# Performance work log

Hardware: AMD Instinct MI355X
Metric: run time of the kernel (lower is better)

## Reference

```python
import jax, jax.numpy as jnp
import numpy as np

B, T, F, H, O = 4096, 64, 512, 64, 2

def setup_inputs() -> dict:
    key = jax.random.key(0)
    ks = jax.random.split(key, 7)
    s_ih = 1.0 / np.sqrt(H)
    return {
        "x": jax.random.normal(ks[0], (B, T, F), dtype=jnp.float32),
        # PyTorch LSTM params: weight_ih_l0 [4H, F], weight_hh_l0 [4H, H], biases [4H]
        "W_ih": jax.random.uniform(ks[1], (4 * H, F), jnp.float32, -s_ih, s_ih),
        "W_hh": jax.random.uniform(ks[2], (4 * H, H), jnp.float32, -s_ih, s_ih),
        "b_ih": jax.random.uniform(ks[3], (4 * H,), jnp.float32, -s_ih, s_ih),
        "b_hh": jax.random.uniform(ks[4], (4 * H,), jnp.float32, -s_ih, s_ih),
        "W_fc": jax.random.uniform(ks[5], (O, H), jnp.float32, -s_ih, s_ih),
        "b_fc": jax.random.uniform(ks[6], (O,), jnp.float32, -s_ih, s_ih),
    }

def _lstm_last_h(x, W_ih, W_hh, b_ih, b_hh):
    # Precompute input contributions for all timesteps: [B, T, 4H]
    xg = jnp.einsum('btf,gf->btg', x, W_ih) + (b_ih + b_hh)
    h0 = jnp.zeros((x.shape[0], W_hh.shape[1]), x.dtype)
    c0 = jnp.zeros_like(h0)

    def step(carry, xt):
        h, c = carry
        gates = xt + h @ W_hh.T  # [B, 4H]
        i, f, g, o = jnp.split(gates, 4, axis=-1)  # PyTorch gate order i,f,g,o
        i = jax.nn.sigmoid(i)
        f = jax.nn.sigmoid(f)
        g = jnp.tanh(g)
        o = jax.nn.sigmoid(o)
        c_new = f * c + i * g
        h_new = o * jnp.tanh(c_new)
        return (h_new, c_new), None

    (hT, _), _ = jax.lax.scan(step, (h0, c0), jnp.swapaxes(xg, 0, 1))  # scan over T
    return hT  # [B, H] = out[:, -1, :]

def reference(x, W_ih, W_hh, b_ih, b_hh, W_fc, b_fc):
    hT = _lstm_last_h(x, W_ih, W_hh, b_ih, b_hh)
    return hT @ W_fc.T + b_fc  # [B, O]
```

## Files before the change

kernel.cpp:

```cpp
#include <hip/hip_runtime.h>

#define B_SZ 4096
#define T_SZ 64
#define F_SZ 512
#define H_SZ 64
#define BR 8
#define TC 8
#define NCHUNK (T_SZ / TC)
#define NTILE 64
#define WIH_HALF_ELEMS (256 * 512)

typedef _Float16 f16x8 __attribute__((ext_vector_type(8)));
typedef float f32x4 __attribute__((ext_vector_type(4)));

__device__ __forceinline__ float fast_rcp(float x) { return __builtin_amdgcn_rcpf(x); }
__device__ __forceinline__ float sigm(float x) { return fast_rcp(1.0f + __expf(-x)); }
__device__ __forceinline__ float tanh_f(float x) {
  x = fminf(15.0f, fmaxf(-15.0f, x));
  float e = __expf(2.0f * x);
  return (e - 1.0f) * fast_rcp(e + 1.0f);
}
__device__ __forceinline__ f16x8 cvt8(float4 a, float4 b) {
  f16x8 h;
  h[0] = (_Float16)a.x; h[1] = (_Float16)a.y; h[2] = (_Float16)a.z; h[3] = (_Float16)a.w;
  h[4] = (_Float16)b.x; h[5] = (_Float16)b.y; h[6] = (_Float16)b.z; h[7] = (_Float16)b.w;
  return h;
}

__global__ void transcode_f16(const float* __restrict__ Wih, const float* __restrict__ Whh,
                              _Float16* __restrict__ ws) {
  const int i4 = (blockIdx.x * 256 + threadIdx.x) * 4;
  if (i4 < WIH_HALF_ELEMS) {
    float4 v = *(const float4*)(Wih + i4);
    ws[i4] = (_Float16)v.x; ws[i4+1] = (_Float16)v.y; ws[i4+2] = (_Float16)v.z; ws[i4+3] = (_Float16)v.w;
  } else {
    const int j4 = i4 - WIH_HALF_ELEMS;
    float4 v = *(const float4*)(Whh + j4);
    _Float16* w2 = ws + WIH_HALF_ELEMS;
    w2[j4] = (_Float16)v.x; w2[j4+1] = (_Float16)v.y; w2[j4+2] = (_Float16)v.z; w2[j4+3] = (_Float16)v.w;
  }
}

__global__ __launch_bounds__(256, 2)
void lstm_fused(const float* __restrict__ x, const _Float16* __restrict__ ws,
                const float* __restrict__ bih, const float* __restrict__ bhh,
                const float* __restrict__ Wfc, const float* __restrict__ bfc,
                float* __restrict__ out)
{
  __shared__ __align__(16) float Ax[4][64 * 64];
  __shared__ __align__(16) _Float16 hbuf[2][8][72];
  __shared__ float cb[8][64];
  __shared__ float h32[8][64];

  const int tid  = threadIdx.x;
  const int wv   = tid >> 6;
  const int lane = tid & 63;
  const int ln   = lane & 15;
  const int kg   = lane >> 4;
  const int br0  = blockIdx.x * BR;
  const int u    = wv * 16 + ln;

  const _Float16* Wihh = ws;
  const _Float16* Whhh = ws + WIH_HALF_ELEMS;

  for (int i = tid; i < 8 * 72; i += 256) (&hbuf[0][0][0])[i] = (_Float16)0.0f;
  for (int i = tid; i < 8 * 64; i += 256) (&cb[0][0])[i] = 0.0f;
  __syncthreads();

  f16x8 whhf[4][2];
  #pragma unroll
  for (int g = 0; g < 4; ++g)
    #pragma unroll
    for (int k2 = 0; k2 < 2; ++k2)
      whhf[g][k2] = *(const f16x8*)(Whhh + (size_t)((g * 4 + wv) * 16 + ln) * H_SZ
                                         + kg * 8 + k2 * 32);

  float bsum[4];
  #pragma unroll
  for (int g = 0; g < 4; ++g) bsum[g] = bih[g * 64 + u] + bhh[g * 64 + u];

  auto issue_tile = [&](int tau) {
    if (tau >= NTILE) return;
    const int cc = tau >> 3, kk = tau & 7, slot = tau & 3;
    #pragma unroll
    for (int j = 0; j < 4; ++j) {
      const int i = wv * 4 + j;
      const int m = i * 4 + (lane >> 4);
      const int kw = (((lane & 15) << 2) ^ ((m & 7) << 2));
      const float* gp = x + (size_t)(br0 + (m & 7)) * (T_SZ * F_SZ)
                          + (size_t)(cc * TC + (m >> 3)) * F_SZ + kk * 64 + kw;
      __builtin_amdgcn_global_load_lds(gp, &Ax[slot][i * 256], 16, 0, 0);
    }
  };

  auto load_bfr = [&](f16x8 (&b)[4][2], int kk) {
    #pragma unroll
    for (int g = 0; g < 4; ++g)
      #pragma unroll
      for (int k2 = 0; k2 < 2; ++k2)
        b[g][k2] = *(const f16x8*)(Wihh + (size_t)((g * 4 + wv) * 16 + ln) * F_SZ
                                        + kk * 64 + kg * 8 + k2 * 32);
  };

  f32x4 acc[4][4];
  const int sw = (ln & 7) << 2;

  auto phaseA_iter = [&](int tau, f16x8 (&bcon)[4][2], f16x8 (&bpre)[4][2]) {
    asm volatile("s_waitcnt vmcnt(16)" ::: "memory");
    __builtin_amdgcn_s_barrier();
    load_bfr(bpre, (tau + 1) & 7);
    issue_tile(tau + 3);
    asm volatile("" ::: "memory");
    const float* axs = &Ax[tau & 3][0];
    #pragma unroll
    for (int t = 0; t < 4; ++t) {
      const int rb  = (t * 16 + ln) * 64;
      const int w00 = (kg * 8) ^ sw;
      float4 a0 = *(const float4*)(axs + rb + w00);
      float4 a1 = *(const float4*)(axs + rb + (w00 ^ 4));
      float4 a2 = *(const float4*)(axs + rb + 32 + w00);
      float4 a3 = *(const float4*)(axs + rb + 32 + (w00 ^ 4));
      f16x8 af0 = cvt8(a0, a1);
      f16x8 af1 = cvt8(a2, a3);
      #pragma unroll
      for (int g = 0; g < 4; ++g) {
        acc[t][g] = __builtin_amdgcn_mfma_f32_16x16x32_f16(af0, bcon[g][0], acc[t][g], 0, 0, 0);
        acc[t][g] = __builtin_amdgcn_mfma_f32_16x16x32_f16(af1, bcon[g][1], acc[t][g], 0, 0, 0);
      }
    }
  };

  issue_tile(0); issue_tile(1); issue_tile(2);
  asm volatile("" ::: "memory");
  f16x8 bA[4][2], bB[4][2];
  load_bfr(bA, 0);

  for (int cc = 0; cc < NCHUNK; ++cc) {
    #pragma unroll
    for (int t = 0; t < 4; ++t)
      #pragma unroll
      for (int g = 0; g < 4; ++g) acc[t][g] = (f32x4){0.0f, 0.0f, 0.0f, 0.0f};

    #pragma unroll
    for (int kp = 0; kp < 4; ++kp) {
      phaseA_iter(cc * 8 + 2 * kp,     bA, bB);
      phaseA_iter(cc * 8 + 2 * kp + 1, bB, bA);
    }

    #pragma unroll
    for (int s = 0; s < TC; ++s) {
      const int st   = cc * TC + s;
      const int half = s & 1;
      f16x8 ah0 = (f16x8){0, 0, 0, 0, 0, 0, 0, 0};
      f16x8 ah1 = (f16x8){0, 0, 0, 0, 0, 0, 0, 0};
      if ((ln >> 3) == half) {
        const _Float16* hr = &hbuf[st & 1][ln & 7][0];
        ah0 = *(const f16x8*)(hr + kg * 8);
        ah1 = *(const f16x8*)(hr + kg * 8 + 32);
      }
      f32x4 gf[4];
      #pragma unroll
      for (int g = 0; g < 4; ++g) {
        gf[g] = __builtin_amdgcn_mfma_f32_16x16x32_f16(ah0, whhf[g][0], acc[s >> 1][g], 0, 0, 0);
        gf[g] = __builtin_amdgcn_mfma_f32_16x16x32_f16(ah1, whhf[g][1], gf[g], 0, 0, 0);
      }
      if ((kg >> 1) == half) {
        const int b0 = (kg & 1) * 4;
        #pragma unroll
        for (int r = 0; r < 4; ++r) {
          const float iv = sigm(gf[0][r] + bsum[0]);
          const float fv = sigm(gf[1][r] + bsum[1]);
          const float gv = tanh_f(gf[2][r] + bsum[2]);
          const float ov = sigm(gf[3][r] + bsum[3]);
          const float cn = fv * cb[b0 + r][u] + iv * gv;
          cb[b0 + r][u] = cn;
          const float hn = ov * tanh_f(cn);
          hbuf[(st + 1) & 1][b0 + r][u] = (_Float16)hn;
          if (st == T_SZ - 1) h32[b0 + r][u] = hn;
        }
      }
      asm volatile("s_waitcnt lgkmcnt(0)" ::: "memory");
      __builtin_amdgcn_s_barrier();
    }
  }

  __syncthreads();
  if (tid < 16) {
    const int r = tid >> 1, j = tid & 1;
    float a = bfc[j];
    #pragma unroll
    for (int uu = 0; uu < 64; ++uu) a += h32[r][uu] * Wfc[j * 64 + uu];
    out[(size_t)(br0 + r) * 2 + j] = a;
  }
}

extern "C" void kernel_launch(void* const* d_in, const int* in_sizes, int n_in,
                              void* d_out, int out_size, void* d_ws, size_t ws_size,
                              hipStream_t stream) {
  const float* x   = (const float*)d_in[0];
  const float* Wih = (const float*)d_in[1];
  const float* Whh = (const float*)d_in[2];
  const float* bih = (const float*)d_in[3];
  const float* bhh = (const float*)d_in[4];
  const float* Wfc = (const float*)d_in[5];
  const float* bfc = (const float*)d_in[6];
  float* out = (float*)d_out;
  _Float16* ws = (_Float16*)d_ws;

  transcode_f16<<<dim3(144), dim3(256), 0, stream>>>(Wih, Whh, ws);
  lstm_fused<<<dim3(B_SZ / BR), dim3(256), 0, stream>>>(x, ws, bih, bhh, Wfc, bfc, out);
}
```

Measured before the change: 207.2 us.

## Split fused LSTM into input-projection GEMM and a separate recurrent scan kernel

Replaces the single fused kernel with two kernels. The first computes the input projection x·W_ih^T plus bias for every batch row and timestep with MFMA and writes it to workspace in fp16, laid out time-major. The second runs the recurrence, prefetching those precomputed gates per 4-step chunk and keeping the cell state in registers. The aim is to take the large GEMM off the serial recurrence path so it runs with full parallelism, at the cost of an extra 128 MB fp16 round trip through HBM and one more launch. The old fused kernel is kept as a fallback for when the workspace is too small.

```diff
diff --git a/kernel.cpp b/kernel.cpp
--- a/kernel.cpp
+++ b/kernel.cpp
@@ -4,12 +4,11 @@
 #define T_SZ 64
 #define F_SZ 512
 #define H_SZ 64
-#define BR 8
-#define TC 8
-#define NCHUNK (T_SZ / TC)
-#define NTILE 64
-#define WIH_HALF_ELEMS (256 * 512)
-
+#define WIH_ELEMS (256 * 512)
+#define WHH_ELEMS (256 * 64)
+#define XG_ELEMS ((size_t)B_SZ * T_SZ * 256)
+
+typedef _Float16 f16x4 __attribute__((ext_vector_type(4)));
 typedef _Float16 f16x8 __attribute__((ext_vector_type(8)));
 typedef float f32x4 __attribute__((ext_vector_type(4)));
 
@@ -30,22 +29,191 @@
 __global__ void transcode_f16(const float* __restrict__ Wih, const float* __restrict__ Whh,
                               _Float16* __restrict__ ws) {
   const int i4 = (blockIdx.x * 256 + threadIdx.x) * 4;
-  if (i4 < WIH_HALF_ELEMS) {
+  if (i4 < WIH_ELEMS) {
     float4 v = *(const float4*)(Wih + i4);
     ws[i4] = (_Float16)v.x; ws[i4+1] = (_Float16)v.y; ws[i4+2] = (_Float16)v.z; ws[i4+3] = (_Float16)v.w;
   } else {
-    const int j4 = i4 - WIH_HALF_ELEMS;
+    const int j4 = i4 - WIH_ELEMS;
     float4 v = *(const float4*)(Whh + j4);
-    _Float16* w2 = ws + WIH_HALF_ELEMS;
+    _Float16* w2 = ws + WIH_ELEMS;
     w2[j4] = (_Float16)v.x; w2[j4+1] = (_Float16)v.y; w2[j4+2] = (_Float16)v.z; w2[j4+3] = (_Float16)v.w;
   }
 }
 
 __global__ __launch_bounds__(256, 2)
-void lstm_fused(const float* __restrict__ x, const _Float16* __restrict__ ws,
-                const float* __restrict__ bih, const float* __restrict__ bhh,
-                const float* __restrict__ Wfc, const float* __restrict__ bfc,
-                float* __restrict__ out)
+void xg_gemm(const float* __restrict__ x, const _Float16* __restrict__ ws,
+             const float* __restrict__ bih, const float* __restrict__ bhh,
+             _Float16* __restrict__ xg)
+{
+  __shared__ __align__(16) _Float16 A[64][520];
+
+  const int tid = threadIdx.x, wv = tid >> 6, lane = tid & 63;
+  const int ln = lane & 15, kg = lane >> 4;
+  const int b = blockIdx.x;
+  const int u = wv * 16 + ln;
+  const _Float16* Wihh = ws;
+
+  {
+    const float* src = x + (size_t)b * (T_SZ * F_SZ) + wv * 8192;
+    #pragma unroll 4
+    for (int i = 0; i < 32; ++i) {
+      float4 v = ((const float4*)src)[i * 64 + lane];
+      f16x4 h = {(_Float16)v.x, (_Float16)v.y, (_Float16)v.z, (_Float16)v.w};
+      const int m = wv * 16 + (i >> 1);
+      const int k = (i & 1) * 256 + lane * 4;
+      *(f16x4*)&A[m][k] = h;
+    }
+  }
+  float bb[4];
+  #pragma unroll
+  for (int g = 0; g < 4; ++g) bb[g] = bih[g * 64 + u] + bhh[g * 64 + u];
+  __syncthreads();
+
+  f32x4 acc[4][4];
+  #pragma unroll
+  for (int mt = 0; mt < 4; ++mt)
+    #pragma unroll
+    for (int g = 0; g < 4; ++g) acc[mt][g] = (f32x4){bb[g], bb[g], bb[g], bb[g]};
+
+  #pragma unroll 2
+  for (int kk = 0; kk < 16; ++kk) {
+    f16x8 bfr[4];
+    #pragma unroll
+    for (int g = 0; g < 4; ++g)
+      bfr[g] = *(const f16x8*)(Wihh + (size_t)((g * 4 + wv) * 16 + ln) * F_SZ + kk * 32 + kg * 8);
+    #pragma unroll
+    for (int mt = 0; mt < 4; ++mt) {
+      f16x8 af = *(const f16x8*)&A[mt * 16 + ln][kk * 32 + kg * 8];
+      #pragma unroll
+      for (int g = 0; g < 4; ++g)
+        acc[mt][g] = __builtin_amdgcn_mfma_f32_16x16x32_f16(af, bfr[g], acc[mt][g], 0, 0, 0);
+    }
+  }
+
+  __syncthreads();
+  _Float16* bn = &A[0][0];
+  #pragma unroll
+  for (int mt = 0; mt < 4; ++mt)
+    #pragma unroll
+    for (int r = 0; r < 4; ++r) {
+      f16x4 p = {(_Float16)acc[mt][0][r], (_Float16)acc[mt][1][r],
+                 (_Float16)acc[mt][2][r], (_Float16)acc[mt][3][r]};
+      *(f16x4*)(bn + (size_t)(mt * 16 + kg * 4 + r) * 264 + u * 4) = p;
+    }
+  __syncthreads();
+  {
+    const int t = tid >> 2, seg = tid & 3;
+    _Float16* dst = xg + ((size_t)t * B_SZ + b) * 256 + seg * 64;
+    const _Float16* srcb = bn + (size_t)t * 264 + seg * 64;
+    #pragma unroll
+    for (int j = 0; j < 8; ++j)
+      *(f16x8*)(dst + j * 8) = *(const f16x8*)(srcb + j * 8);
+  }
+}
+
+__global__ __launch_bounds__(256, 2)
+void lstm_scan(const _Float16* __restrict__ xg, const _Float16* __restrict__ ws,
+               const float* __restrict__ Wfc, const float* __restrict__ bfc,
+               float* __restrict__ out)
+{
+  __shared__ __align__(16) _Float16 Xs[2][4][8][264];
+  __shared__ __align__(16) _Float16 hbuf[2][8][72];
+  __shared__ float h32[8][64];
+
+  const int tid = threadIdx.x, wv = tid >> 6, lane = tid & 63;
+  const int ln = lane & 15, kg = lane >> 4;
+  const int br0 = blockIdx.x * 8;
+  const int u = wv * 16 + ln;
+  const _Float16* Whhh = ws + WIH_ELEMS;
+
+  for (int i = tid; i < 2 * 8 * 72; i += 256) (&hbuf[0][0][0])[i] = (_Float16)0.0f;
+
+  f16x8 whhf[4][2];
+  #pragma unroll
+  for (int g = 0; g < 4; ++g)
+    #pragma unroll
+    for (int k2 = 0; k2 < 2; ++k2)
+      whhf[g][k2] = *(const f16x8*)(Whhh + (size_t)((g * 4 + wv) * 16 + ln) * H_SZ
+                                         + kg * 8 + k2 * 32);
+
+  f32x4 cst = {0.0f, 0.0f, 0.0f, 0.0f};
+
+  uint4 pf[4];
+  {
+    const _Float16* gsrc = xg + ((size_t)(0 * 4 + wv) * B_SZ + br0) * 256;
+    #pragma unroll
+    for (int i = 0; i < 4; ++i) pf[i] = *(const uint4*)(gsrc + (i * 64 + lane) * 8);
+  }
+  __syncthreads();
+
+  for (int c = 0; c < 16; ++c) {
+    #pragma unroll
+    for (int i = 0; i < 4; ++i)
+      *(uint4*)&Xs[c & 1][wv][i * 2 + (lane >> 5)][(lane & 31) * 8] = pf[i];
+    {
+      const int cn = c < 15 ? c + 1 : 15;
+      const _Float16* gsrc = xg + ((size_t)(cn * 4 + wv) * B_SZ + br0) * 256;
+      #pragma unroll
+      for (int i = 0; i < 4; ++i) pf[i] = *(const uint4*)(gsrc + (i * 64 + lane) * 8);
+    }
+    __syncthreads();
+
+    #pragma unroll
+    for (int sl = 0; sl < 4; ++sl) {
+      const int st = c * 4 + sl;
+      const _Float16* hr = &hbuf[st & 1][ln & 7][0];
+      f16x8 ah0 = *(const f16x8*)(hr + kg * 8);
+      f16x8 ah1 = *(const f16x8*)(hr + kg * 8 + 32);
+      f32x4 gf[4];
+      if (kg < 2) {
+        f16x4 xv[4];
+        #pragma unroll
+        for (int r = 0; r < 4; ++r)
+          xv[r] = *(const f16x4*)&Xs[c & 1][sl][kg * 4 + r][u * 4];
+        #pragma unroll
+        for (int g = 0; g < 4; ++g)
+          gf[g] = (f32x4){(float)xv[0][g], (float)xv[1][g], (float)xv[2][g], (float)xv[3][g]};
+      } else {
+        #pragma unroll
+        for (int g = 0; g < 4; ++g) gf[g] = (f32x4){0.0f, 0.0f, 0.0f, 0.0f};
+      }
+      #pragma unroll
+      for (int g = 0; g < 4; ++g) {
+        gf[g] = __builtin_amdgcn_mfma_f32_16x16x32_f16(ah0, whhf[g][0], gf[g], 0, 0, 0);
+        gf[g] = __builtin_amdgcn_mfma_f32_16x16x32_f16(ah1, whhf[g][1], gf[g], 0, 0, 0);
+      }
+      if (kg < 2) {
+        #pragma unroll
+        for (int r = 0; r < 4; ++r) {
+          const float iv = sigm(gf[0][r]);
+          const float fv = sigm(gf[1][r]);
+          const float gv = tanh_f(gf[2][r]);
+          const float ov = sigm(gf[3][r]);
+          const float cn = fv * cst[r] + iv * gv;
+          cst[r] = cn;
+          const float hn = ov * tanh_f(cn);
+          hbuf[(st + 1) & 1][kg * 4 + r][u] = (_Float16)hn;
+          if (st == T_SZ - 1) h32[kg * 4 + r][u] = hn;
+        }
+      }
+      __syncthreads();
+    }
+  }
+
+  if (tid < 16) {
+    const int r = tid >> 1, j = tid & 1;
+    float a = bfc[j];
+    #pragma unroll
+    for (int uu = 0; uu < 64; ++uu) a += h32[r][uu] * Wfc[j * 64 + uu];
+    out[(size_t)(br0 + r) * 2 + j] = a;
+  }
+}
+
+__global__ __launch_bounds__(256, 2)
+void lstm_fused_fb(const float* __restrict__ x, const _Float16* __restrict__ ws,
+                   const float* __restrict__ bih, const float* __restrict__ bhh,
+                   const float* __restrict__ Wfc, const float* __restrict__ bfc,
+                   float* __restrict__ out)
 {
   __shared__ __align__(16) float Ax[4][64 * 64];
   __shared__ __align__(16) _Float16 hbuf[2][8][72];
@@ -57,11 +225,11 @@
   const int lane = tid & 63;
   const int ln   = lane & 15;
   const int kg   = lane >> 4;
-  const int br0  = blockIdx.x * BR;
+  const int br0  = blockIdx.x * 8;
   const int u    = wv * 16 + ln;
 
   const _Float16* Wihh = ws;
-  const _Float16* Whhh = ws + WIH_HALF_ELEMS;
+  const _Float16* Whhh = ws + WIH_ELEMS;
 
   for (int i = tid; i < 8 * 72; i += 256) (&hbuf[0][0][0])[i] = (_Float16)0.0f;
   for (int i = tid; i < 8 * 64; i += 256) (&cb[0][0])[i] = 0.0f;
@@ -80,7 +248,7 @@
   for (int g = 0; g < 4; ++g) bsum[g] = bih[g * 64 + u] + bhh[g * 64 + u];
 
   auto issue_tile = [&](int tau) {
-    if (tau >= NTILE) return;
+    if (tau >= 64) return;
     const int cc = tau >> 3, kk = tau & 7, slot = tau & 3;
     #pragma unroll
     for (int j = 0; j < 4; ++j) {
@@ -88,18 +256,17 @@
       const int m = i * 4 + (lane >> 4);
       const int kw = (((lane & 15) << 2) ^ ((m & 7) << 2));
       const float* gp = x + (size_t)(br0 + (m & 7)) * (T_SZ * F_SZ)
-                          + (size_t)(cc * TC + (m >> 3)) * F_SZ + kk * 64 + kw;
+                          + (size_t)(cc * 8 + (m >> 3)) * F_SZ + kk * 64 + kw;
       __builtin_amdgcn_global_load_lds(gp, &Ax[slot][i * 256], 16, 0, 0);
     }
   };
-
-  auto load_bfr = [&](f16x8 (&b)[4][2], int kk) {
+  auto load_bfr = [&](f16x8 (&bf)[4][2], int kk) {
     #pragma unroll
     for (int g = 0; g < 4; ++g)
       #pragma unroll
       for (int k2 = 0; k2 < 2; ++k2)
-        b[g][k2] = *(const f16x8*)(Wihh + (size_t)((g * 4 + wv) * 16 + ln) * F_SZ
-                                        + kk * 64 + kg * 8 + k2 * 32);
+        bf[g][k2] = *(const f16x8*)(Wihh + (size_t)((g * 4 + wv) * 16 + ln) * F_SZ
+                                         + kk * 64 + kg * 8 + k2 * 32);
   };
 
   f32x4 acc[4][4];
@@ -135,7 +302,7 @@
   f16x8 bA[4][2], bB[4][2];
   load_bfr(bA, 0);
 
-  for (int cc = 0; cc < NCHUNK; ++cc) {
+  for (int cc = 0; cc < 8; ++cc) {
     #pragma unroll
     for (int t = 0; t < 4; ++t)
       #pragma unroll
@@ -148,8 +315,8 @@
     }
 
     #pragma unroll
-    for (int s = 0; s < TC; ++s) {
-      const int st   = cc * TC + s;
+    for (int s = 0; s < 8; ++s) {
+      const int st   = cc * 8 + s;
       const int half = s & 1;
       f16x8 ah0 = (f16x8){0, 0, 0, 0, 0, 0, 0, 0};
       f16x8 ah1 = (f16x8){0, 0, 0, 0, 0, 0, 0, 0};
@@ -208,5 +375,13 @@
   _Float16* ws = (_Float16*)d_ws;
 
   transcode_f16<<<dim3(144), dim3(256), 0, stream>>>(Wih, Whh, ws);
-  lstm_fused<<<dim3(B_SZ / BR), dim3(256), 0, stream>>>(x, ws, bih, bhh, Wfc, bfc, out);
-}
+
+  const size_t need = (size_t)(WIH_ELEMS + WHH_ELEMS) * 2 + XG_ELEMS * 2;
+  if (ws_size >= need) {
+    _Float16* xg = ws + WIH_ELEMS + WHH_ELEMS;
+    xg_gemm<<<dim3(B_SZ), dim3(256), 0, stream>>>(x, ws, bih, bhh, xg);
+    lstm_scan<<<dim3(B_SZ / 8), dim3(256), 0, stream>>>(xg, ws, Wfc, bfc, out);
+  } else {
+    lstm_fused_fb<<<dim3(B_SZ / 8), dim3(256), 0, stream>>>(x, ws, bih, bhh, Wfc, bfc, out);
+  }
+}
```

New measurement: 341.5 us. 64.8% more time.
